# Optimization experiments

Measured on AMD Instinct MI355X. Metric: run time of the kernel, lower is better.

The kernel has to match this reference:

```python
import jax, jax.numpy as jnp
import numpy as np
from math import sqrt

D_MODEL = 1024
N_HEADS = 16
D_V = D_MODEL // N_HEADS
D_FF = 4 * D_MODEL
EPS = 1e-5


def setup_inputs() -> dict:
    key = jax.random.key(0)
    ks = jax.random.split(key, 12)
    N, L = 2, 2048
    s = 0.02
    return {
        'queries': jax.random.normal(ks[0], (N, L, D_MODEL), jnp.float32),
        'keys': jax.random.normal(ks[1], (N, L, D_MODEL), jnp.float32),
        'values': jax.random.normal(ks[2], (N, L, D_MODEL), jnp.float32),
        'mask': jnp.ones((N, 1, 1, L), jnp.int32),
        'fc_w': jax.random.normal(ks[3], (D_MODEL, D_MODEL), jnp.float32) * s,
        'fc_b': jnp.zeros((D_MODEL,), jnp.float32),
        'ln1_g': jnp.ones((D_MODEL,), jnp.float32),
        'ln1_b': jnp.zeros((D_MODEL,), jnp.float32),
        'ff_w1': jax.random.normal(ks[4], (D_MODEL, D_FF), jnp.float32) * s,
        'ff_b1': jnp.zeros((D_FF,), jnp.float32),
        'ff_w2': jax.random.normal(ks[5], (D_FF, D_MODEL), jnp.float32) * s,
        'ff_b2': jnp.zeros((D_MODEL,), jnp.float32),
        'ln2_g': jnp.ones((D_MODEL,), jnp.float32),
        'ln2_b': jnp.zeros((D_MODEL,), jnp.float32),
    }


def layer_norm(x, g, b):
    mu = jnp.mean(x, axis=-1, keepdims=True)
    var = jnp.mean(jnp.square(x - mu), axis=-1, keepdims=True)
    return (x - mu) * jax.lax.rsqrt(var + EPS) * g + b


def reference(queries, keys, values, mask, fc_w, fc_b, ln1_g, ln1_b,
              ff_w1, ff_b1, ff_w2, ff_b2, ln2_g, ln2_b):
    N, Lq, _ = queries.shape
    Lk = keys.shape[1]
    # NOTE: the original module never applies its Q/K/V linear layers; raw
    # inputs are reshaped directly into heads.
    q = queries.reshape(N, Lq, N_HEADS, D_V).transpose(0, 2, 1, 3)  # nhqd
    k = keys.reshape(N, Lk, N_HEADS, D_V)                           # nlhd
    v = values.reshape(N, Lk, N_HEADS, D_V)                         # nlhd
    energy = jnp.einsum('nhqd,nlhd->nhql', q, k)
    energy = jnp.where(mask == 0, -jnp.inf, energy)
    # original scales by sqrt(d_model), not sqrt(d_v)
    attn = jax.nn.softmax(energy / sqrt(D_MODEL), axis=-1)
    out = jnp.einsum('nhql,nlhd->nqhd', attn, v).reshape(N, Lq, D_MODEL)
    attention = out @ fc_w + fc_b
    x1 = layer_norm(attention + queries, ln1_g, ln1_b)
    fc = jax.nn.relu(x1 @ ff_w1 + ff_b1) @ ff_w2 + ff_b2
    x2 = layer_norm(fc + x1, ln2_g, ln2_b)
    return x2
```

## Files before the change

### kernel.cpp

```cpp
#include <hip/hip_runtime.h>
#include <stdint.h>

typedef unsigned short u16;
typedef __bf16 bf16x8 __attribute__((ext_vector_type(8), may_alias));
typedef float f32x4 __attribute__((ext_vector_type(4), may_alias));

typedef void __attribute__((address_space(1))) as1_void;
typedef void __attribute__((address_space(3))) as3_void;

#define MFMA16 __builtin_amdgcn_mfma_f32_16x16x32_bf16

__device__ __forceinline__ void async_copy16(const void* g, void* l) {
    __builtin_amdgcn_global_load_lds((as1_void*)g, (as3_void*)l, 16, 0, 0);
}

__device__ __forceinline__ u16 f2bf(float f) {
    union { float f; unsigned u; } c; c.f = f;
    unsigned u = c.u;
    u += 0x7fffu + ((u >> 16) & 1u);
    return (u16)(u >> 16);
}

__global__ __launch_bounds__(256) void cast_f32_bf16(
    const float* __restrict__ in, u16* __restrict__ out, int n4, float scale) {
    int i = blockIdx.x * 256 + threadIdx.x;
    if (i < n4) {
        f32x4 v = *(const f32x4*)&in[(size_t)i * 4];
        ushort4 o;
        o.x = f2bf(v[0] * scale); o.y = f2bf(v[1] * scale);
        o.z = f2bf(v[2] * scale); o.w = f2bf(v[3] * scale);
        *(ushort4*)&out[(size_t)i * 4] = o;
    }
}

__global__ __launch_bounds__(256) void transpose_cast(
    const float* __restrict__ in, u16* __restrict__ out, int R, int C) {
    __shared__ float tile[64][65];
    const float* inb = in + (size_t)blockIdx.z * R * C;
    u16* outb = out + (size_t)blockIdx.z * R * C;
    int t = threadIdx.x;
    int c0 = blockIdx.x * 64, r0 = blockIdx.y * 64;
    int tr = t >> 4, tc = (t & 15) * 4;
#pragma unroll
    for (int p = 0; p < 4; ++p) {
        int r = tr + p * 16;
        f32x4 v = *(const f32x4*)&inb[(size_t)(r0 + r) * C + c0 + tc];
        tile[r][tc] = v[0]; tile[r][tc + 1] = v[1];
        tile[r][tc + 2] = v[2]; tile[r][tc + 3] = v[3];
    }
    __syncthreads();
    int wc = t >> 4, wr = (t & 15) * 4;
#pragma unroll
    for (int p = 0; p < 4; ++p) {
        int cl = wc + p * 16;
        ushort4 o;
        o.x = f2bf(tile[wr + 0][cl]); o.y = f2bf(tile[wr + 1][cl]);
        o.z = f2bf(tile[wr + 2][cl]); o.w = f2bf(tile[wr + 3][cl]);
        *(ushort4*)&outb[(size_t)(c0 + cl) * R + r0 + wr] = o;
    }
}

__global__ __launch_bounds__(256) void flash_attn(
    const u16* __restrict__ Q, const u16* __restrict__ Kb,
    const u16* __restrict__ VT, const int* __restrict__ mask,
    u16* __restrict__ O) {
    __shared__ u16 kls[2][8192];
    __shared__ u16 vls[8192];
    __shared__ u16 pls[8][2048];

    const int bid = blockIdx.x;
    const int qt = bid & 15;
    const int h = (bid >> 4) & 15;
    const int n = bid >> 8;
    const int t = threadIdx.x;
    const int w = t >> 6, lane = t & 63;
    const int m16 = lane & 15, quad = lane >> 4;

    const size_t qrowA = (size_t)(n * 2048 + qt * 128 + w * 16 + m16);
    const size_t qrowB = qrowA + 64;
    bf16x8 qfA0 = *(const bf16x8*)&Q[qrowA * 1024 + h * 64 + quad * 8];
    bf16x8 qfA1 = *(const bf16x8*)&Q[qrowA * 1024 + h * 64 + 32 + quad * 8];
    bf16x8 qfB0 = *(const bf16x8*)&Q[qrowB * 1024 + h * 64 + quad * 8];
    bf16x8 qfB1 = *(const bf16x8*)&Q[qrowB * 1024 + h * 64 + 32 + quad * 8];

    const int* maskn = mask + n * 2048;
    int allones;
    {
        int ok = 1;
#pragma unroll
        for (int i = 0; i < 8; ++i) {
            int4 mv = *(const int4*)&maskn[lane * 32 + i * 4];
            ok &= (mv.x != 0) & (mv.y != 0) & (mv.z != 0) & (mv.w != 0);
        }
        allones = __all(ok);
    }

    f32x4 otA[4] = {}, otB[4] = {};
    f32x4 sumA = {}, sumB = {};

    const u16* Kbase = Kb + (size_t)(n * 2048) * 1024 + h * 64;
    const u16* Vbase = VT + (size_t)(n * 1024 + h * 64) * 2048;
    u16* pwA = &pls[w * 2][0];
    u16* pwB = &pls[w * 2 + 1][0];

#pragma unroll
    for (int i = 0; i < 4; ++i) {
        int e = w * 4 + i;
        async_copy16(&Kbase[(size_t)((e >> 1) * 16 + m16) * 1024 + (e & 1) * 32 + quad * 8],
                     &kls[0][e * 512]);
    }
    __syncthreads();

    for (int kt = 0; kt < 16; ++kt) {
        const u16* kcur = kls[kt & 1];
        if (kt + 1 < 16) {
            u16* knext = kls[(kt + 1) & 1];
#pragma unroll
            for (int i = 0; i < 4; ++i) {
                int e = w * 4 + i;
                async_copy16(&Kbase[(size_t)((kt + 1) * 128 + (e >> 1) * 16 + m16) * 1024 +
                                    (e & 1) * 32 + quad * 8], &knext[e * 512]);
            }
        }
#pragma unroll
        for (int i = 0; i < 4; ++i) {
            int e = w * 4 + i;
            async_copy16(&Vbase[(size_t)((e >> 2) * 16 + m16) * 2048 + kt * 128 +
                                (e & 3) * 32 + quad * 8], &vls[e * 512]);
        }

        f32x4 sA[8] = {}, sB[8] = {};
#pragma unroll
        for (int ct = 0; ct < 8; ++ct) {
            bf16x8 a0 = *(const bf16x8*)&kcur[(ct * 2 + 0) * 512 + lane * 8];
            bf16x8 a1 = *(const bf16x8*)&kcur[(ct * 2 + 1) * 512 + lane * 8];
            sA[ct] = MFMA16(a0, qfA0, sA[ct], 0, 0, 0);
            sA[ct] = MFMA16(a1, qfA1, sA[ct], 0, 0, 0);
            sB[ct] = MFMA16(a0, qfB0, sB[ct], 0, 0, 0);
            sB[ct] = MFMA16(a1, qfB1, sB[ct], 0, 0, 0);
        }

        if (allones) {
#pragma unroll
            for (int ct = 0; ct < 8; ++ct) {
                int c = ct * 2 + (quad >> 1);
                int off = m16 * 128 + (((c ^ m16) & 15) << 3) + (quad & 1) * 4;
                {
                    float p0 = __builtin_amdgcn_exp2f(sA[ct][0]);
                    float p1 = __builtin_amdgcn_exp2f(sA[ct][1]);
                    float p2 = __builtin_amdgcn_exp2f(sA[ct][2]);
                    float p3 = __builtin_amdgcn_exp2f(sA[ct][3]);
                    sumA[0] += p0; sumA[1] += p1; sumA[2] += p2; sumA[3] += p3;
                    unsigned lo = __builtin_amdgcn_perm(__float_as_uint(p1), __float_as_uint(p0), 0x07060302);
                    unsigned hi = __builtin_amdgcn_perm(__float_as_uint(p3), __float_as_uint(p2), 0x07060302);
                    *(uint2*)&pwA[off] = make_uint2(lo, hi);
                }
                {
                    float p0 = __builtin_amdgcn_exp2f(sB[ct][0]);
                    float p1 = __builtin_amdgcn_exp2f(sB[ct][1]);
                    float p2 = __builtin_amdgcn_exp2f(sB[ct][2]);
                    float p3 = __builtin_amdgcn_exp2f(sB[ct][3]);
                    sumB[0] += p0; sumB[1] += p1; sumB[2] += p2; sumB[3] += p3;
                    unsigned lo = __builtin_amdgcn_perm(__float_as_uint(p1), __float_as_uint(p0), 0x07060302);
                    unsigned hi = __builtin_amdgcn_perm(__float_as_uint(p3), __float_as_uint(p2), 0x07060302);
                    *(uint2*)&pwB[off] = make_uint2(lo, hi);
                }
            }
        } else {
#pragma unroll
            for (int ct = 0; ct < 8; ++ct) {
                const int4 mv = *(const int4*)&maskn[kt * 128 + ct * 16 + quad * 4];
                int c = ct * 2 + (quad >> 1);
                int off = m16 * 128 + (((c ^ m16) & 15) << 3) + (quad & 1) * 4;
                {
                    float p0 = __builtin_amdgcn_exp2f(sA[ct][0]) * (mv.x ? 1.f : 0.f);
                    float p1 = __builtin_amdgcn_exp2f(sA[ct][1]) * (mv.y ? 1.f : 0.f);
                    float p2 = __builtin_amdgcn_exp2f(sA[ct][2]) * (mv.z ? 1.f : 0.f);
                    float p3 = __builtin_amdgcn_exp2f(sA[ct][3]) * (mv.w ? 1.f : 0.f);
                    sumA[0] += p0; sumA[1] += p1; sumA[2] += p2; sumA[3] += p3;
                    unsigned lo = __builtin_amdgcn_perm(__float_as_uint(p1), __float_as_uint(p0), 0x07060302);
                    unsigned hi = __builtin_amdgcn_perm(__float_as_uint(p3), __float_as_uint(p2), 0x07060302);
                    *(uint2*)&pwA[off] = make_uint2(lo, hi);
                }
                {
                    float p0 = __builtin_amdgcn_exp2f(sB[ct][0]) * (mv.x ? 1.f : 0.f);
                    float p1 = __builtin_amdgcn_exp2f(sB[ct][1]) * (mv.y ? 1.f : 0.f);
                    float p2 = __builtin_amdgcn_exp2f(sB[ct][2]) * (mv.z ? 1.f : 0.f);
                    float p3 = __builtin_amdgcn_exp2f(sB[ct][3]) * (mv.w ? 1.f : 0.f);
                    sumB[0] += p0; sumB[1] += p1; sumB[2] += p2; sumB[3] += p3;
                    unsigned lo = __builtin_amdgcn_perm(__float_as_uint(p1), __float_as_uint(p0), 0x07060302);
                    unsigned hi = __builtin_amdgcn_perm(__float_as_uint(p3), __float_as_uint(p2), 0x07060302);
                    *(uint2*)&pwB[off] = make_uint2(lo, hi);
                }
            }
        }

        __syncthreads();

        bf16x8 pfA[4], pfB[4];
#pragma unroll
        for (int kc2 = 0; kc2 < 4; ++kc2) {
            int off = m16 * 128 + ((((kc2 * 4 + quad) ^ m16) & 15) << 3);
            pfA[kc2] = *(const bf16x8*)&pwA[off];
            pfB[kc2] = *(const bf16x8*)&pwB[off];
        }
#pragma unroll
        for (int kc2 = 0; kc2 < 4; ++kc2) {
#pragma unroll
            for (int dt = 0; dt < 4; ++dt) {
                bf16x8 vf = *(const bf16x8*)&vls[(dt * 4 + kc2) * 512 + lane * 8];
                otA[dt] = MFMA16(vf, pfA[kc2], otA[dt], 0, 0, 0);
                otB[dt] = MFMA16(vf, pfB[kc2], otB[dt], 0, 0, 0);
            }
        }
        __syncthreads();
    }

    float lA = (sumA[0] + sumA[1]) + (sumA[2] + sumA[3]);
    float lB = (sumB[0] + sumB[1]) + (sumB[2] + sumB[3]);
    lA += __shfl_xor(lA, 16); lA += __shfl_xor(lA, 32);
    lB += __shfl_xor(lB, 16); lB += __shfl_xor(lB, 32);
    float invA = 1.f / fmaxf(lA, 1e-30f);
    float invB = 1.f / fmaxf(lB, 1e-30f);

    const size_t obA = qrowA * 1024 + h * 64;
    const size_t obB = qrowB * 1024 + h * 64;
#pragma unroll
    for (int dt = 0; dt < 4; ++dt) {
        unsigned lo = (unsigned)f2bf(otA[dt][0] * invA) | ((unsigned)f2bf(otA[dt][1] * invA) << 16);
        unsigned hi = (unsigned)f2bf(otA[dt][2] * invA) | ((unsigned)f2bf(otA[dt][3] * invA) << 16);
        *(uint2*)&O[obA + dt * 16 + quad * 4] = make_uint2(lo, hi);
        lo = (unsigned)f2bf(otB[dt][0] * invB) | ((unsigned)f2bf(otB[dt][1] * invB) << 16);
        hi = (unsigned)f2bf(otB[dt][2] * invB) | ((unsigned)f2bf(otB[dt][3] * invB) << 16);
        *(uint2*)&O[obB + dt * 16 + quad * 4] = make_uint2(lo, hi);
    }
}

template <int BM, int BN, int RELU, int OUTBF>
__global__ __launch_bounds__(256) void gemm_bt(
    const u16* __restrict__ A, const u16* __restrict__ Bt,
    const float* __restrict__ bias, void* __restrict__ Cout,
    int M, int N, int K) {
    constexpr int MI = BM / 32;
    constexpr int NJ = BN / 32;
    __shared__ u16 sm[2][(BM + BN) * 64];
    const int lane = threadIdx.x & 63;
    const int w = threadIdx.x >> 6;
    const int m16 = lane & 15, quad = lane >> 4;
    const int nBn = N / BN;
    const int bm = blockIdx.x / nBn, bn = blockIdx.x % nBn;
    const int r2 = w >> 1, c2 = w & 1;

    const u16* Abase = A + (size_t)(bm * BM + m16) * K + quad * 8;
    const u16* Bbase = Bt + (size_t)(bn * BN + m16) * K + quad * 8;

    auto stage = [&](int buf, int k0) {
        u16* smA = &sm[buf][0];
        u16* smB = smA + BM * 64;
#pragma unroll
        for (int i = 0; i < MI; ++i) {
            int e = w * MI + i;
            async_copy16(&Abase[(size_t)((e >> 1) * 16) * K + k0 + (e & 1) * 32], &smA[e * 512]);
        }
#pragma unroll
        for (int i = 0; i < NJ; ++i) {
            int e = w * NJ + i;
            async_copy16(&Bbase[(size_t)((e >> 1) * 16) * K + k0 + (e & 1) * 32], &smB[e * 512]);
        }
    };

    f32x4 acc[MI][NJ] = {};
    const int nK = K >> 6;
    stage(0, 0);
    __syncthreads();
    for (int kt = 0; kt < nK; ++kt) {
        if (kt + 1 < nK) stage((kt + 1) & 1, (kt + 1) << 6);
        const u16* smA = &sm[kt & 1][0];
        const u16* smB = smA + BM * 64;
#pragma unroll
        for (int kc = 0; kc < 2; ++kc) {
            bf16x8 a[MI], b[NJ];
#pragma unroll
            for (int i = 0; i < MI; ++i)
                a[i] = *(const bf16x8*)&smA[((r2 * MI + i) * 2 + kc) * 512 + lane * 8];
#pragma unroll
            for (int j = 0; j < NJ; ++j)
                b[j] = *(const bf16x8*)&smB[((c2 * NJ + j) * 2 + kc) * 512 + lane * 8];
#pragma unroll
            for (int i = 0; i < MI; ++i)
#pragma unroll
                for (int j = 0; j < NJ; ++j)
                    acc[i][j] = MFMA16(a[i], b[j], acc[i][j], 0, 0, 0);
        }
        __syncthreads();
    }
    float bv[NJ];
#pragma unroll
    for (int j = 0; j < NJ; ++j)
        bv[j] = bias[bn * BN + c2 * (BN / 2) + j * 16 + m16];
#pragma unroll
    for (int i = 0; i < MI; ++i) {
        int row0 = bm * BM + r2 * (BM / 2) + i * 16 + quad * 4;
#pragma unroll
        for (int j = 0; j < NJ; ++j) {
            int col = bn * BN + c2 * (BN / 2) + j * 16 + m16;
#pragma unroll
            for (int r = 0; r < 4; ++r) {
                float v = acc[i][j][r] + bv[j];
                if (RELU) v = fmaxf(v, 0.f);
                size_t idx = (size_t)(row0 + r) * N + col;
                if (OUTBF) ((u16*)Cout)[idx] = f2bf(v);
                else ((float*)Cout)[idx] = v;
            }
        }
    }
}

__global__ __launch_bounds__(256) void ln_residual(
    const float* __restrict__ x, const float* __restrict__ res,
    const float* __restrict__ g, const float* __restrict__ b,
    float* __restrict__ out_f32, u16* __restrict__ out_bf16) {
    __shared__ float smr[8];
    int row = blockIdx.x;
    int t = threadIdx.x;
    f32x4 xv = *(const f32x4*)&x[(size_t)row * 1024 + t * 4];
    f32x4 rv = *(const f32x4*)&res[(size_t)row * 1024 + t * 4];
    xv += rv;
    float s = xv[0] + xv[1] + xv[2] + xv[3];
    float ss = xv[0] * xv[0] + xv[1] * xv[1] + xv[2] * xv[2] + xv[3] * xv[3];
#pragma unroll
    for (int d = 1; d < 64; d <<= 1) {
        s += __shfl_xor(s, d);
        ss += __shfl_xor(ss, d);
    }
    int w = t >> 6, lane = t & 63;
    if (lane == 0) { smr[w] = s; smr[4 + w] = ss; }
    __syncthreads();
    s = smr[0] + smr[1] + smr[2] + smr[3];
    ss = smr[4] + smr[5] + smr[6] + smr[7];
    float mu = s * (1.f / 1024.f);
    float var = ss * (1.f / 1024.f) - mu * mu;
    float rs = rsqrtf(var + 1e-5f);
    f32x4 gv = *(const f32x4*)&g[t * 4];
    f32x4 bv = *(const f32x4*)&b[t * 4];
    f32x4 y;
#pragma unroll
    for (int i = 0; i < 4; ++i) y[i] = (xv[i] - mu) * rs * gv[i] + bv[i];
    *(f32x4*)&out_f32[(size_t)row * 1024 + t * 4] = y;
    if (out_bf16) {
        ushort4 o;
        o.x = f2bf(y[0]); o.y = f2bf(y[1]); o.z = f2bf(y[2]); o.w = f2bf(y[3]);
        *(ushort4*)&out_bf16[(size_t)row * 1024 + t * 4] = o;
    }
}

extern "C" void kernel_launch(void* const* d_in, const int* in_sizes, int n_in,
                              void* d_out, int out_size, void* d_ws, size_t ws_size,
                              hipStream_t stream) {
    const float* q = (const float*)d_in[0];
    const float* k = (const float*)d_in[1];
    const float* v = (const float*)d_in[2];
    const int* mask = (const int*)d_in[3];
    const float* fc_b = (const float*)d_in[5];
    const float* ln1_g = (const float*)d_in[6];
    const float* ln1_b = (const float*)d_in[7];
    const float* ff_b1 = (const float*)d_in[9];
    const float* ff_b2 = (const float*)d_in[11];
    const float* ln2_g = (const float*)d_in[12];
    const float* ln2_b = (const float*)d_in[13];
    const float* fc_w = (const float*)d_in[4];
    const float* ff_w1 = (const float*)d_in[8];
    const float* ff_w2 = (const float*)d_in[10];

    char* ws = (char*)d_ws;
    const size_t MB = 1024 * 1024;
    u16* qbf = (u16*)(ws + 0);
    u16* kbf = (u16*)(ws + 8 * MB);
    u16* vT  = (u16*)(ws + 16 * MB);
    u16* ao  = (u16*)(ws + 24 * MB);
    u16* hbuf = (u16*)(ws + 0);
    u16* fcwT = (u16*)(ws + 32 * MB);
    u16* w1T  = (u16*)(ws + 34 * MB);
    u16* w2T  = (u16*)(ws + 42 * MB);
    float* attn_raw = (float*)(ws + 50 * MB);
    float* fc_raw   = (float*)(ws + 50 * MB);
    float* x1   = (float*)(ws + 66 * MB);
    u16* x1bf   = (u16*)(ws + 82 * MB);

    const float k2 = 0.03125f * 1.44269504088896340736f;

    cast_f32_bf16<<<4096, 256, 0, stream>>>(q, qbf, 1048576, k2);
    cast_f32_bf16<<<4096, 256, 0, stream>>>(k, kbf, 1048576, 1.0f);
    transpose_cast<<<dim3(16, 32, 2), 256, 0, stream>>>(v, vT, 2048, 1024);
    transpose_cast<<<dim3(16, 16, 1), 256, 0, stream>>>(fc_w, fcwT, 1024, 1024);
    transpose_cast<<<dim3(64, 16, 1), 256, 0, stream>>>(ff_w1, w1T, 1024, 4096);
    transpose_cast<<<dim3(16, 64, 1), 256, 0, stream>>>(ff_w2, w2T, 4096, 1024);

    flash_attn<<<512, 256, 0, stream>>>(qbf, kbf, vT, mask, ao);

    gemm_bt<64, 128, 0, 0><<<64 * 8, 256, 0, stream>>>(ao, fcwT, fc_b, attn_raw, 4096, 1024, 1024);
    ln_residual<<<4096, 256, 0, stream>>>(attn_raw, q, ln1_g, ln1_b, x1, x1bf);

    gemm_bt<128, 128, 1, 1><<<32 * 32, 256, 0, stream>>>(x1bf, w1T, ff_b1, hbuf, 4096, 4096, 1024);
    gemm_bt<64, 128, 0, 0><<<64 * 8, 256, 0, stream>>>(hbuf, w2T, ff_b2, fc_raw, 4096, 1024, 4096);
    ln_residual<<<4096, 256, 0, stream>>>(fc_raw, x1, ln2_g, ln2_b, (float*)d_out, (u16*)nullptr);
}
```

Measured before the change: 405.3 us.

## Split-K the N=1024 GEMMs with 128x128 tiles, summing partials in layernorm

Adds a SPLITK template parameter to the bf16 GEMM. The attention output projection and the FFN down-projection now run with 128x128 tiles and two K slices, so the grid stays at 512 blocks while each tile gets more reuse. The second slice writes its partial sum to a separate fp32 buffer, and the residual layernorm kernel reads and adds it. The FFN path only uses split-K when the workspace is large enough. The cost is an extra 16MB fp32 partial buffer written and read per GEMM.

```diff
diff --git a/kernel.cpp b/kernel.cpp
--- a/kernel.cpp
+++ b/kernel.cpp
@@ -236,11 +236,11 @@
     }
 }
 
-template <int BM, int BN, int RELU, int OUTBF>
+template <int BM, int BN, int RELU, int OUTBF, int SPLITK>
 __global__ __launch_bounds__(256) void gemm_bt(
     const u16* __restrict__ A, const u16* __restrict__ Bt,
     const float* __restrict__ bias, void* __restrict__ Cout,
-    int M, int N, int K) {
+    void* __restrict__ Cout1, int M, int N, int K) {
     constexpr int MI = BM / 32;
     constexpr int NJ = BN / 32;
     __shared__ u16 sm[2][(BM + BN) * 64];
@@ -248,8 +248,17 @@
     const int w = threadIdx.x >> 6;
     const int m16 = lane & 15, quad = lane >> 4;
     const int nBn = N / BN;
-    const int bm = blockIdx.x / nBn, bn = blockIdx.x % nBn;
+    int bid = blockIdx.x;
+    int slice = 0;
+    if (SPLITK > 1) {
+        const int nblk = (M / BM) * nBn;
+        slice = bid / nblk;
+        bid = bid - slice * nblk;
+    }
+    const int bm = bid / nBn, bn = bid % nBn;
     const int r2 = w >> 1, c2 = w & 1;
+    const int Ks = K / SPLITK;
+    const int kOff = slice * Ks;
 
     const u16* Abase = A + (size_t)(bm * BM + m16) * K + quad * 8;
     const u16* Bbase = Bt + (size_t)(bn * BN + m16) * K + quad * 8;
@@ -270,11 +279,11 @@
     };
 
     f32x4 acc[MI][NJ] = {};
-    const int nK = K >> 6;
-    stage(0, 0);
+    const int nK = Ks >> 6;
+    stage(0, kOff);
     __syncthreads();
     for (int kt = 0; kt < nK; ++kt) {
-        if (kt + 1 < nK) stage((kt + 1) & 1, (kt + 1) << 6);
+        if (kt + 1 < nK) stage((kt + 1) & 1, kOff + ((kt + 1) << 6));
         const u16* smA = &sm[kt & 1][0];
         const u16* smB = smA + BM * 64;
 #pragma unroll
@@ -297,7 +306,9 @@
     float bv[NJ];
 #pragma unroll
     for (int j = 0; j < NJ; ++j)
-        bv[j] = bias[bn * BN + c2 * (BN / 2) + j * 16 + m16];
+        bv[j] = (SPLITK == 1 || slice == 0)
+                    ? bias[bn * BN + c2 * (BN / 2) + j * 16 + m16] : 0.f;
+    void* Csel = (SPLITK > 1 && slice != 0) ? Cout1 : Cout;
 #pragma unroll
     for (int i = 0; i < MI; ++i) {
         int row0 = bm * BM + r2 * (BM / 2) + i * 16 + quad * 4;
@@ -309,15 +320,16 @@
                 float v = acc[i][j][r] + bv[j];
                 if (RELU) v = fmaxf(v, 0.f);
                 size_t idx = (size_t)(row0 + r) * N + col;
-                if (OUTBF) ((u16*)Cout)[idx] = f2bf(v);
-                else ((float*)Cout)[idx] = v;
+                if (OUTBF) ((u16*)Csel)[idx] = f2bf(v);
+                else ((float*)Csel)[idx] = v;
             }
         }
     }
 }
 
 __global__ __launch_bounds__(256) void ln_residual(
-    const float* __restrict__ x, const float* __restrict__ res,
+    const float* __restrict__ x, const float* __restrict__ x2,
+    const float* __restrict__ res,
     const float* __restrict__ g, const float* __restrict__ b,
     float* __restrict__ out_f32, u16* __restrict__ out_bf16) {
     __shared__ float smr[8];
@@ -326,6 +338,10 @@
     f32x4 xv = *(const f32x4*)&x[(size_t)row * 1024 + t * 4];
     f32x4 rv = *(const f32x4*)&res[(size_t)row * 1024 + t * 4];
     xv += rv;
+    if (x2) {
+        f32x4 pv = *(const f32x4*)&x2[(size_t)row * 1024 + t * 4];
+        xv += pv;
+    }
     float s = xv[0] + xv[1] + xv[2] + xv[3];
     float ss = xv[0] * xv[0] + xv[1] * xv[1] + xv[2] * xv[2] + xv[3] * xv[3];
 #pragma unroll
@@ -386,6 +402,9 @@
     float* fc_raw   = (float*)(ws + 50 * MB);
     float* x1   = (float*)(ws + 66 * MB);
     u16* x1bf   = (u16*)(ws + 82 * MB);
+    float* attn_rawB = (float*)(ws + 0);
+    float* fcB = (float*)(ws + 90 * MB);
+    const bool big = ws_size >= 106 * MB;
 
     const float k2 = 0.03125f * 1.44269504088896340736f;
 
@@ -398,10 +417,22 @@
 
     flash_attn<<<512, 256, 0, stream>>>(qbf, kbf, vT, mask, ao);
 
-    gemm_bt<64, 128, 0, 0><<<64 * 8, 256, 0, stream>>>(ao, fcwT, fc_b, attn_raw, 4096, 1024, 1024);
-    ln_residual<<<4096, 256, 0, stream>>>(attn_raw, q, ln1_g, ln1_b, x1, x1bf);
-
-    gemm_bt<128, 128, 1, 1><<<32 * 32, 256, 0, stream>>>(x1bf, w1T, ff_b1, hbuf, 4096, 4096, 1024);
-    gemm_bt<64, 128, 0, 0><<<64 * 8, 256, 0, stream>>>(hbuf, w2T, ff_b2, fc_raw, 4096, 1024, 4096);
-    ln_residual<<<4096, 256, 0, stream>>>(fc_raw, x1, ln2_g, ln2_b, (float*)d_out, (u16*)nullptr);
-}
+    gemm_bt<128, 128, 0, 0, 2><<<32 * 8 * 2, 256, 0, stream>>>(
+        ao, fcwT, fc_b, attn_raw, attn_rawB, 4096, 1024, 1024);
+    ln_residual<<<4096, 256, 0, stream>>>(attn_raw, attn_rawB, q, ln1_g, ln1_b, x1, x1bf);
+
+    gemm_bt<128, 128, 1, 1, 1><<<32 * 32, 256, 0, stream>>>(
+        x1bf, w1T, ff_b1, hbuf, nullptr, 4096, 4096, 1024);
+
+    if (big) {
+        gemm_bt<128, 128, 0, 0, 2><<<32 * 8 * 2, 256, 0, stream>>>(
+            hbuf, w2T, ff_b2, fc_raw, fcB, 4096, 1024, 4096);
+        ln_residual<<<4096, 256, 0, stream>>>(fc_raw, fcB, x1, ln2_g, ln2_b,
+                                              (float*)d_out, (u16*)nullptr);
+    } else {
+        gemm_bt<64, 128, 0, 0, 1><<<64 * 8, 256, 0, stream>>>(
+            hbuf, w2T, ff_b2, fc_raw, nullptr, 4096, 1024, 4096);
+        ln_residual<<<4096, 256, 0, stream>>>(fc_raw, nullptr, x1, ln2_g, ln2_b,
+                                              (float*)d_out, (u16*)nullptr);
+    }
+}
```

After: 385.9 us. -4.8%, faster.
